# Optimization experiments

Measured on AMD Instinct MI355X. Metric: run time of the kernel, lower is better.

Reference implementation:

```python
import jax, jax.numpy as jnp
import numpy as np
from jax import lax

B, L = 2, 1024
D_MODEL, D_STATE, EXPAND, D_CONV = 1024, 16, 2, 4
D_INNER = EXPAND * D_MODEL            # 2048
DT_RANK = (D_MODEL + 15) // 16        # 64


def setup_inputs() -> dict:
    key = jax.random.key(0)
    ks = jax.random.split(key, 8)
    g = lambda k, shape, s=0.02: jax.random.normal(k, shape, dtype=jnp.float32) * s
    # Mamba-style A init: A = -exp(A_log), A_log = log(1..d_state) per channel
    A_log = jnp.log(jnp.broadcast_to(
        jnp.arange(1, D_STATE + 1, dtype=jnp.float32), (D_INNER, D_STATE)))
    return {
        "x": jax.random.normal(ks[0], (B, L, D_MODEL), dtype=jnp.float32),
        "W_in": g(ks[1], (D_MODEL, 2 * D_INNER)),
        "conv_w": g(ks[2], (D_INNER, D_CONV), 0.1),
        "conv_b": jnp.zeros((D_INNER,), jnp.float32),
        "W_x": g(ks[3], (D_INNER, DT_RANK + 2 * D_STATE)),
        "W_dt": g(ks[4], (DT_RANK, D_INNER)),
        "b_dt": g(ks[5], (D_INNER,), 0.1),
        "A_log": A_log,
        "D_skip": jnp.ones((D_INNER,), jnp.float32),
        "W_out": g(ks[6], (D_INNER, D_MODEL)),
    }


def reference(x, W_in, conv_w, conv_b, W_x, W_dt, b_dt, A_log, D_skip, W_out):
    # in_proj -> (u, z): [B, L, D_INNER] each
    xz = x @ W_in
    u, z = xz[..., :D_INNER], xz[..., D_INNER:]

    # causal depthwise conv1d, kernel D_CONV (small fixed loop over taps)
    up = jnp.pad(u, ((0, 0), (D_CONV - 1, 0), (0, 0)))
    u = sum(up[:, k:k + L, :] * conv_w[:, k] for k in range(D_CONV)) + conv_b
    u = jax.nn.silu(u)

    # input-dependent dt, B, C
    x_dbl = u @ W_x                                    # [B, L, dt_rank + 2N]
    dt = x_dbl[..., :DT_RANK]
    Bm = x_dbl[..., DT_RANK:DT_RANK + D_STATE]         # [B, L, N]
    Cm = x_dbl[..., DT_RANK + D_STATE:]                # [B, L, N]
    delta = jax.nn.softplus(dt @ W_dt + b_dt)          # [B, L, D]

    A = -jnp.exp(A_log)                                # [D, N]
    deltaA = jnp.exp(jnp.einsum('bld,dn->bldn', delta, A))   # [B, L, D, N]
    dBu = (delta * u)[..., None] * Bm[:, :, None, :]          # [B, L, D, N]

    def step(h, inp):
        dA_t, dBu_t, c_t = inp                         # [B,D,N],[B,D,N],[B,N]
        h = dA_t * h + dBu_t
        y_t = jnp.einsum('bdn,bn->bd', h, c_t)
        return h, y_t

    h0 = jnp.zeros((B, D_INNER, D_STATE), x.dtype)
    _, ys = lax.scan(step, h0,
                     (deltaA.transpose(1, 0, 2, 3),
                      dBu.transpose(1, 0, 2, 3),
                      Cm.transpose(1, 0, 2)))
    y = ys.transpose(1, 0, 2) + u * D_skip             # [B, L, D_INNER]
    y = y * jax.nn.silu(z)                             # gated output
    return y @ W_out                                   # [B, L, D_MODEL]
```

## Files before the change

### kernel.cpp

```cpp
#include <hip/hip_runtime.h>


typedef unsigned short u16;
typedef unsigned int   u32;

#define B_SZ 2
#define L_SZ 1024
#define DM   1024
#define DI   2048
#define DS   16
#define DTR  64
#define NXD  96
#define NCHUNK 16
#define CL   64
#define KSPLIT 8
#define KC     256
#define OSPLIT 4

typedef __bf16 bf16x8 __attribute__((ext_vector_type(8)));
typedef float  f32x4  __attribute__((ext_vector_type(4)));

__device__ __forceinline__ u16 f2bf(float f) {
    u32 x = __float_as_uint(f);
    x += 0x7fffu + ((x >> 16) & 1u);
    return (u16)(x >> 16);
}

__device__ __forceinline__ void gld_lds16(const u16* g, u16* l) {
    __builtin_amdgcn_global_load_lds(
        (const __attribute__((address_space(1))) u32*)g,
        (__attribute__((address_space(3))) u32*)l, 16, 0, 0);
}

__global__ __launch_bounds__(256) void gemm128u2(
    const u16* __restrict__ A, const u16* __restrict__ BT,
    float* __restrict__ C, const float* __restrict__ bias,
    int M, int N, int K, int KCHUNK, int op)
{
    __shared__ u16 As0[128 * 32];
    __shared__ u16 Bs0[128 * 32];
    __shared__ u16 As1[128 * 32];
    __shared__ u16 Bs1[128 * 32];

    const int tid  = threadIdx.x;
    const int wave = tid >> 6;
    const int lane = tid & 63;
    const int q    = lane >> 4;
    const int r16  = lane & 15;
    const int wm   = (wave & 1) * 64;
    const int wn   = (wave >> 1) * 64;
    const int m0   = blockIdx.y * 128;
    const int n0   = blockIdx.x * 128;
    const int srow = tid >> 2;
    const int sseg = (tid & 3) * 8;
    const int kb   = blockIdx.z * KCHUNK;

    const u16* gA0 = A  + (size_t)(m0 + srow)      * K + sseg;
    const u16* gA1 = A  + (size_t)(m0 + 64 + srow) * K + sseg;
    const u16* gB0 = BT + (size_t)(n0 + srow)      * K + sseg;
    const u16* gB1 = BT + (size_t)(n0 + 64 + srow) * K + sseg;
    u16* lA0 = As0 + tid * 8;  u16* lA0b = As0 + 2048 + tid * 8;
    u16* lB0 = Bs0 + tid * 8;  u16* lB0b = Bs0 + 2048 + tid * 8;
    u16* lA1 = As1 + tid * 8;  u16* lA1b = As1 + 2048 + tid * 8;
    u16* lB1 = Bs1 + tid * 8;  u16* lB1b = Bs1 + 2048 + tid * 8;

    f32x4 acc[4][4];
#pragma unroll
    for (int s = 0; s < 4; ++s)
#pragma unroll
        for (int j = 0; j < 4; ++j) acc[s][j] = (f32x4){0.f, 0.f, 0.f, 0.f};

    for (int k0 = kb; k0 < kb + KCHUNK; k0 += 64) {
        __syncthreads();
        gld_lds16(gA0 + k0, lA0);
        gld_lds16(gA1 + k0, lA0b);
        gld_lds16(gB0 + k0, lB0);
        gld_lds16(gB1 + k0, lB0b);
        gld_lds16(gA0 + k0 + 32, lA1);
        gld_lds16(gA1 + k0 + 32, lA1b);
        gld_lds16(gB0 + k0 + 32, lB1);
        gld_lds16(gB1 + k0 + 32, lB1b);
        __syncthreads();

        bf16x8 af[4], bfr[4];
#pragma unroll
        for (int s = 0; s < 4; ++s)
            af[s] = *(const bf16x8*)(As0 + (wm + s * 16 + r16) * 32 + q * 8);
#pragma unroll
        for (int j = 0; j < 4; ++j)
            bfr[j] = *(const bf16x8*)(Bs0 + (wn + j * 16 + r16) * 32 + q * 8);
#pragma unroll
        for (int s = 0; s < 4; ++s)
#pragma unroll
            for (int j = 0; j < 4; ++j)
                acc[s][j] = __builtin_amdgcn_mfma_f32_16x16x32_bf16(
                    af[s], bfr[j], acc[s][j], 0, 0, 0);
#pragma unroll
        for (int s = 0; s < 4; ++s)
            af[s] = *(const bf16x8*)(As1 + (wm + s * 16 + r16) * 32 + q * 8);
#pragma unroll
        for (int j = 0; j < 4; ++j)
            bfr[j] = *(const bf16x8*)(Bs1 + (wn + j * 16 + r16) * 32 + q * 8);
#pragma unroll
        for (int s = 0; s < 4; ++s)
#pragma unroll
            for (int j = 0; j < 4; ++j)
                acc[s][j] = __builtin_amdgcn_mfma_f32_16x16x32_bf16(
                    af[s], bfr[j], acc[s][j], 0, 0, 0);
    }

    float* Cz = C + (size_t)blockIdx.z * M * N;
#pragma unroll
    for (int s = 0; s < 4; ++s) {
        const int row0 = m0 + wm + s * 16 + q * 4;
#pragma unroll
        for (int j = 0; j < 4; ++j) {
            const int col = n0 + wn + j * 16 + r16;
            if (op == 1) {
                const float bv = bias[col];
#pragma unroll
                for (int i = 0; i < 4; ++i) {
                    float v = acc[s][j][i] + bv;
                    v = (v > 20.f) ? v : log1pf(__expf(v));
                    Cz[(size_t)(row0 + i) * N + col] = v;
                }
            } else {
#pragma unroll
                for (int i = 0; i < 4; ++i)
                    Cz[(size_t)(row0 + i) * N + col] = acc[s][j][i];
            }
        }
    }
}

__global__ __launch_bounds__(256) void reduce_out(
    const float* __restrict__ part, float* __restrict__ out, int n)
{
    const int i = (blockIdx.x * 256 + threadIdx.x) * 4;
    if (i >= n) return;
    f32x4 v = *(const f32x4*)(part + i);
#pragma unroll
    for (int s = 1; s < OSPLIT; ++s) {
        f32x4 p = *(const f32x4*)(part + (size_t)s * n + i);
        v.x += p.x; v.y += p.y; v.z += p.z; v.w += p.w;
    }
    *(f32x4*)(out + i) = v;
}

__global__ __launch_bounds__(256) void gemm_skinny_splitk(
    const u16* __restrict__ A, const u16* __restrict__ BT,
    float* __restrict__ Cpart, int M, int N, int K)
{
    constexpr int LDT = 40;
    __shared__ u16 As[128 * LDT];
    __shared__ u16 Bs[64 * LDT];

    const int tid  = threadIdx.x;
    const int wave = tid >> 6;
    const int lane = tid & 63;
    const int q    = lane >> 4;
    const int r16  = lane & 15;
    const int m0   = blockIdx.y * 128;
    const int n0   = blockIdx.x * 64;
    const int kcs  = blockIdx.z * KC;
    const int sr   = tid >> 2;
    const int ss   = (tid & 3) * 8;

    f32x4 acc[2][4];
#pragma unroll
    for (int s = 0; s < 2; ++s)
#pragma unroll
        for (int j = 0; j < 4; ++j) acc[s][j] = (f32x4){0.f, 0.f, 0.f, 0.f};

    const int  bcol   = n0 + sr;
    const bool bvalid = bcol < N;

    for (int k0 = kcs; k0 < kcs + KC; k0 += 32) {
        __syncthreads();
        uint4 a0 = *(const uint4*)(A + (size_t)(m0 + sr)      * K + k0 + ss);
        uint4 a1 = *(const uint4*)(A + (size_t)(m0 + 64 + sr) * K + k0 + ss);
        uint4 bv = make_uint4(0u, 0u, 0u, 0u);
        if (bvalid) bv = *(const uint4*)(BT + (size_t)bcol * K + k0 + ss);
        *(uint4*)(As + sr * LDT + ss)        = a0;
        *(uint4*)(As + (64 + sr) * LDT + ss) = a1;
        *(uint4*)(Bs + sr * LDT + ss)        = bv;
        __syncthreads();

        bf16x8 af[2], bfr[4];
#pragma unroll
        for (int s = 0; s < 2; ++s)
            af[s] = *(const bf16x8*)(As + (wave * 32 + s * 16 + r16) * LDT + q * 8);
#pragma unroll
        for (int j = 0; j < 4; ++j)
            bfr[j] = *(const bf16x8*)(Bs + (j * 16 + r16) * LDT + q * 8);
#pragma unroll
        for (int s = 0; s < 2; ++s)
#pragma unroll
            for (int j = 0; j < 4; ++j)
                acc[s][j] = __builtin_amdgcn_mfma_f32_16x16x32_bf16(
                    af[s], bfr[j], acc[s][j], 0, 0, 0);
    }

    float* Cp = Cpart + (size_t)blockIdx.z * M * N;
#pragma unroll
    for (int s = 0; s < 2; ++s) {
        const int row0 = m0 + wave * 32 + s * 16 + q * 4;
#pragma unroll
        for (int j = 0; j < 4; ++j) {
            const int col = n0 + j * 16 + r16;
            if (col < N) {
#pragma unroll
                for (int i = 0; i < 4; ++i)
                    Cp[(size_t)(row0 + i) * N + col] = acc[s][j][i];
            }
        }
    }
}

__global__ __launch_bounds__(256) void reduce_xdbl(
    const float* __restrict__ part, float* __restrict__ xdbl,
    u16* __restrict__ dtbf)
{
    const int i = blockIdx.x * 256 + threadIdx.x;
    const int row = i / NXD, col = i - row * NXD;
    float v = 0.f;
#pragma unroll
    for (int s = 0; s < KSPLIT; ++s)
        v += part[(size_t)s * (B_SZ * L_SZ * NXD) + i];
    xdbl[i] = v;
    if (col < DTR) dtbf[row * DTR + col] = f2bf(v);
}

__device__ __forceinline__ void tr_tile(
    const float* __restrict__ in, u16* __restrict__ out,
    int R, int C, int tr, int tc, int tid, float (*t)[33])
{
    const int tx = tid & 31, ty = tid >> 5;
    const int r0 = tr * 32, c0 = tc * 32;
#pragma unroll
    for (int i = 0; i < 4; ++i) {
        int r = r0 + ty + i * 8, c = c0 + tx;
        if (r < R && c < C) t[ty + i * 8][tx] = in[(size_t)r * C + c];
    }
    __syncthreads();
#pragma unroll
    for (int i = 0; i < 4; ++i) {
        int oR = c0 + ty + i * 8, oC = r0 + tx;
        if (oR < C && oC < R) out[(size_t)oR * R + oC] = f2bf(t[tx][ty + i * 8]);
    }
}

__global__ __launch_bounds__(256) void prep_kernel(
    const float* __restrict__ x,     u16* __restrict__ xbf,
    const float* __restrict__ W_in,  u16* __restrict__ winT,
    const float* __restrict__ W_out, u16* __restrict__ woutT,
    const float* __restrict__ W_x,   u16* __restrict__ wxT,
    const float* __restrict__ W_dt,  u16* __restrict__ wdtT)
{
    __shared__ float t[32][33];
    const int id  = blockIdx.x;
    const int tid = threadIdx.x;
    if (id < 4096) {
        tr_tile(W_in, winT, 1024, 4096, id >> 7, id & 127, tid, t);
    } else if (id < 6144) {
        int i2 = id - 4096;
        tr_tile(W_out, woutT, 2048, 1024, i2 >> 5, i2 & 31, tid, t);
    } else if (id < 6336) {
        int i3 = id - 6144;
        tr_tile(W_x, wxT, 2048, 96, i3 / 3, i3 % 3, tid, t);
    } else if (id < 6464) {
        int i4 = id - 6336;
        tr_tile(W_dt, wdtT, 64, 2048, i4 >> 6, i4 & 63, tid, t);
    } else {
        int i = (id - 6464) * 256 + tid;
        xbf[i] = f2bf(x[i]);
    }
}

__global__ __launch_bounds__(256) void conv_silu_kernel(
    const float* __restrict__ xz, const float* __restrict__ cw,
    const float* __restrict__ cb, float* __restrict__ uc, u16* __restrict__ ucbf)
{
    const int idx = blockIdx.x * 256 + threadIdx.x;
    const int d   = idx & (DI - 1);
    const int pos = idx >> 11;
    const int l   = pos & (L_SZ - 1);
    float s = cb[d];
#pragma unroll
    for (int k = 0; k < 4; ++k) {
        int ls = l + k - 3;
        if (ls >= 0)
            s = fmaf(xz[(size_t)(pos + k - 3) * (2 * DI) + d], cw[d * 4 + k], s);
    }
    float v = s / (1.f + __expf(-s));
    uc[idx]   = v;
    ucbf[idx] = f2bf(v);
}

__global__ __launch_bounds__(256) void scan_pass1(
    const float* __restrict__ delta, const float* __restrict__ uc,
    const float* __restrict__ xdbl, const float* __restrict__ A_log,
    float* __restrict__ hbuf, float* __restrict__ pbuf)
{
    const int c = blockIdx.x;
    const int d = blockIdx.y * 256 + threadIdx.x;
    const int b = blockIdx.z;
    float Av[16], h[16], P[16];
#pragma unroll
    for (int n = 0; n < 16; ++n) {
        Av[n] = -__expf(A_log[d * 16 + n]);
        h[n] = 0.f; P[n] = 1.f;
    }
    const int rowbase = b * L_SZ + c * CL;
    for (int i = 0; i < CL; ++i) {
        const int row = rowbase + i;
        float dlt = delta[(size_t)row * DI + d];
        float uu  = uc[(size_t)row * DI + d];
        float du  = dlt * uu;
        const float* xr = xdbl + (size_t)row * NXD;
#pragma unroll
        for (int n = 0; n < 16; ++n) {
            float e = __expf(dlt * Av[n]);
            P[n] *= e;
            h[n] = fmaf(e, h[n], du * xr[DTR + n]);
        }
    }
    size_t base = ((size_t)((b * NCHUNK + c) * DI + d)) * 16;
#pragma unroll
    for (int n = 0; n < 16; ++n) { hbuf[base + n] = h[n]; pbuf[base + n] = P[n]; }
}

__global__ __launch_bounds__(256) void scan_pass2(
    float* __restrict__ hbuf, const float* __restrict__ pbuf)
{
    const int j = blockIdx.x * 256 + threadIdx.x;
    const int b = blockIdx.y;
    float h0 = 0.f;
    for (int cc = 0; cc < NCHUNK; ++cc) {
        size_t o = ((size_t)(b * NCHUNK + cc)) * (DI * 16) + j;
        float hl = hbuf[o];
        float Pl = pbuf[o];
        hbuf[o] = h0;
        h0 = fmaf(Pl, h0, hl);
    }
}

__global__ __launch_bounds__(256) void scan_pass3(
    const float* __restrict__ delta, const float* __restrict__ uc,
    const float* __restrict__ xdbl, const float* __restrict__ A_log,
    const float* __restrict__ hbuf, const float* __restrict__ xz,
    const float* __restrict__ Dskip, u16* __restrict__ ybf)
{
    const int c = blockIdx.x;
    const int d = blockIdx.y * 256 + threadIdx.x;
    const int b = blockIdx.z;
    float Av[16], h[16];
    size_t base = ((size_t)((b * NCHUNK + c) * DI + d)) * 16;
#pragma unroll
    for (int n = 0; n < 16; ++n) {
        Av[n] = -__expf(A_log[d * 16 + n]);
        h[n]  = hbuf[base + n];
    }
    const float Dk = Dskip[d];
    const int rowbase = b * L_SZ + c * CL;
    for (int i = 0; i < CL; ++i) {
        const int row = rowbase + i;
        float dlt = delta[(size_t)row * DI + d];
        float uu  = uc[(size_t)row * DI + d];
        float du  = dlt * uu;
        const float* xr = xdbl + (size_t)row * NXD;
        float y = 0.f;
#pragma unroll
        for (int n = 0; n < 16; ++n) {
            float e = __expf(dlt * Av[n]);
            h[n] = fmaf(e, h[n], du * xr[DTR + n]);
            y = fmaf(h[n], xr[DTR + DS + n], y);
        }
        float zz = xz[(size_t)row * (2 * DI) + DI + d];
        float yv = fmaf(uu, Dk, y) * (zz / (1.f + __expf(-zz)));
        ybf[(size_t)row * DI + d] = f2bf(yv);
    }
}

constexpr size_t OFF_XZ      = 0;
constexpr size_t OFF_UC      = OFF_XZ    + 8388608;
constexpr size_t OFF_DELTA   = OFF_UC    + 4194304;
constexpr size_t OFF_XDBL    = OFF_DELTA + 4194304;
constexpr size_t OFF_SCRATCH = OFF_XDBL  + 196608;
constexpr size_t OFF_F32_END = OFF_SCRATCH + 4194304;
constexpr size_t SOFF_XBF   = 0;
constexpr size_t SOFF_WINT  = SOFF_XBF   + 2097152;
constexpr size_t SOFF_UCBF  = SOFF_WINT  + 4194304;
constexpr size_t SOFF_WXT   = SOFF_UCBF  + 4194304;
constexpr size_t SOFF_DTBF  = SOFF_WXT   + 196608;
constexpr size_t SOFF_WDTT  = SOFF_DTBF  + 131072;
constexpr size_t SOFF_WOUTT = SOFF_WDTT  + 131072;
constexpr size_t SOFF_YBF   = SOFF_WOUTT + 2097152;

extern "C" void kernel_launch(void* const* d_in, const int* in_sizes, int n_in,
                              void* d_out, int out_size, void* d_ws, size_t ws_size,
                              hipStream_t stream)
{
    const float* x     = (const float*)d_in[0];
    const float* W_in  = (const float*)d_in[1];
    const float* cw    = (const float*)d_in[2];
    const float* cb    = (const float*)d_in[3];
    const float* W_x   = (const float*)d_in[4];
    const float* W_dt  = (const float*)d_in[5];
    const float* b_dt  = (const float*)d_in[6];
    const float* A_log = (const float*)d_in[7];
    const float* Dsk   = (const float*)d_in[8];
    const float* W_out = (const float*)d_in[9];
    float* out = (float*)d_out;

    float* wsf   = (float*)d_ws;
    float* xz    = wsf + OFF_XZ;
    float* opart = wsf + OFF_XZ;
    float* uc    = wsf + OFF_UC;
    float* dlt   = wsf + OFF_DELTA;
    float* xdbl  = wsf + OFF_XDBL;
    float* xpart = wsf + OFF_SCRATCH;
    float* hbuf  = wsf + OFF_SCRATCH;
    float* pbuf  = wsf + OFF_SCRATCH + 2097152;
    u16* sb    = (u16*)(wsf + OFF_F32_END);
    u16* xbf   = sb + SOFF_XBF;
    u16* winT  = sb + SOFF_WINT;
    u16* ucbf  = sb + SOFF_UCBF;
    u16* wxT   = sb + SOFF_WXT;
    u16* dtbf  = sb + SOFF_DTBF;
    u16* wdtT  = sb + SOFF_WDTT;
    u16* woutT = sb + SOFF_WOUTT;
    u16* ybf   = sb + SOFF_YBF;

    prep_kernel<<<14656, 256, 0, stream>>>(x, xbf, W_in, winT, W_out, woutT,
                                           W_x, wxT, W_dt, wdtT);

    gemm128u2<<<dim3(4096 / 128, 2048 / 128, 1), 256, 0, stream>>>(
        xbf, winT, xz, nullptr, 2048, 4096, 1024, 1024, 0);

    conv_silu_kernel<<<(B_SZ * L_SZ * DI) / 256, 256, 0, stream>>>(xz, cw, cb, uc, ucbf);

    gemm_skinny_splitk<<<dim3(2, 2048 / 128, KSPLIT), 256, 0, stream>>>(
        ucbf, wxT, xpart, 2048, NXD, 2048);
    reduce_xdbl<<<(B_SZ * L_SZ * NXD) / 256, 256, 0, stream>>>(xpart, xdbl, dtbf);

    gemm128u2<<<dim3(2048 / 128, 2048 / 128, 1), 256, 0, stream>>>(
        dtbf, wdtT, dlt, b_dt, 2048, 2048, 64, 64, 1);

    scan_pass1<<<dim3(NCHUNK, DI / 256, B_SZ), 256, 0, stream>>>(dlt, uc, xdbl, A_log, hbuf, pbuf);
    scan_pass2<<<dim3(DI * 16 / 256, B_SZ), 256, 0, stream>>>(hbuf, pbuf);
    scan_pass3<<<dim3(NCHUNK, DI / 256, B_SZ), 256, 0, stream>>>(dlt, uc, xdbl, A_log, hbuf, xz, Dsk, ybf);

    gemm128u2<<<dim3(1024 / 128, 2048 / 128, OSPLIT), 256, 0, stream>>>(
        ybf, woutT, opart, nullptr, 2048, 1024, 2048, 2048 / OSPLIT, 0);
    reduce_out<<<(2048 * 1024 / 4 + 255) / 256, 256, 0, stream>>>(
        opart, out, 2048 * 1024);
}
```

Before: 278.8 us.

## Fuse three-pass chunked scan with decoupled lookback and store xz, u in bf16

Merges the three scan kernels into one, where each chunk block waits on a flag from the previous chunk and reads its carried state. This removes the separate carry-propagation kernel, one recomputation launch, and the hbuf/pbuf round trips. The in_proj GEMM now writes xz as bf16, and the fp32 copy of the conv output is dropped, so the scan reads bf16 u and z, roughly halving that traffic. The cost is a serial dependency across the 16 chunks, which could deadlock if blocks are not scheduled in order, plus lower precision for u and z.

Result: slower. 679.9 us (+143.9%).

```diff
diff --git a/kernel.cpp b/kernel.cpp
--- a/kernel.cpp
+++ b/kernel.cpp
@@ -25,6 +25,9 @@
     x += 0x7fffu + ((x >> 16) & 1u);
     return (u16)(x >> 16);
 }
+__device__ __forceinline__ float bf2f(u16 v) {
+    return __uint_as_float(((u32)v) << 16);
+}
 
 __device__ __forceinline__ void gld_lds16(const u16* g, u16* l) {
     __builtin_amdgcn_global_load_lds(
@@ -34,7 +37,8 @@
 
 __global__ __launch_bounds__(256) void gemm128u2(
     const u16* __restrict__ A, const u16* __restrict__ BT,
-    float* __restrict__ C, const float* __restrict__ bias,
+    float* __restrict__ Cf, u16* __restrict__ Cb,
+    const float* __restrict__ bias,
     int M, int N, int K, int KCHUNK, int op)
 {
     __shared__ u16 As0[128 * 32];
@@ -109,25 +113,29 @@
                     af[s], bfr[j], acc[s][j], 0, 0, 0);
     }
 
-    float* Cz = C + (size_t)blockIdx.z * M * N;
 #pragma unroll
     for (int s = 0; s < 4; ++s) {
         const int row0 = m0 + wm + s * 16 + q * 4;
 #pragma unroll
         for (int j = 0; j < 4; ++j) {
             const int col = n0 + wn + j * 16 + r16;
-            if (op == 1) {
+            if (op == 0) {
+                float* Cz = Cf + (size_t)blockIdx.z * M * N;
+#pragma unroll
+                for (int i = 0; i < 4; ++i)
+                    Cz[(size_t)(row0 + i) * N + col] = acc[s][j][i];
+            } else if (op == 1) {
                 const float bv = bias[col];
 #pragma unroll
                 for (int i = 0; i < 4; ++i) {
                     float v = acc[s][j][i] + bv;
                     v = (v > 20.f) ? v : log1pf(__expf(v));
-                    Cz[(size_t)(row0 + i) * N + col] = v;
+                    Cf[(size_t)(row0 + i) * N + col] = v;
                 }
             } else {
 #pragma unroll
                 for (int i = 0; i < 4; ++i)
-                    Cz[(size_t)(row0 + i) * N + col] = acc[s][j][i];
+                    Cb[(size_t)(row0 + i) * N + col] = f2bf(acc[s][j][i]);
             }
         }
     }
@@ -255,7 +263,8 @@
     const float* __restrict__ W_in,  u16* __restrict__ winT,
     const float* __restrict__ W_out, u16* __restrict__ woutT,
     const float* __restrict__ W_x,   u16* __restrict__ wxT,
-    const float* __restrict__ W_dt,  u16* __restrict__ wdtT)
+    const float* __restrict__ W_dt,  u16* __restrict__ wdtT,
+    int* __restrict__ flags)
 {
     __shared__ float t[32][33];
     const int id  = blockIdx.x;
@@ -271,15 +280,17 @@
     } else if (id < 6464) {
         int i4 = id - 6336;
         tr_tile(W_dt, wdtT, 64, 2048, i4 >> 6, i4 & 63, tid, t);
-    } else {
+    } else if (id < 14656) {
         int i = (id - 6464) * 256 + tid;
         xbf[i] = f2bf(x[i]);
+    } else {
+        flags[tid] = 0;
     }
 }
 
 __global__ __launch_bounds__(256) void conv_silu_kernel(
-    const float* __restrict__ xz, const float* __restrict__ cw,
-    const float* __restrict__ cb, float* __restrict__ uc, u16* __restrict__ ucbf)
+    const u16* __restrict__ xzbf, const float* __restrict__ cw,
+    const float* __restrict__ cb, u16* __restrict__ ucbf)
 {
     const int idx = blockIdx.x * 256 + threadIdx.x;
     const int d   = idx & (DI - 1);
@@ -290,32 +301,38 @@
     for (int k = 0; k < 4; ++k) {
         int ls = l + k - 3;
         if (ls >= 0)
-            s = fmaf(xz[(size_t)(pos + k - 3) * (2 * DI) + d], cw[d * 4 + k], s);
+            s = fmaf(bf2f(xzbf[(size_t)(pos + k - 3) * (2 * DI) + d]), cw[d * 4 + k], s);
     }
     float v = s / (1.f + __expf(-s));
-    uc[idx]   = v;
     ucbf[idx] = f2bf(v);
 }
 
-__global__ __launch_bounds__(256) void scan_pass1(
-    const float* __restrict__ delta, const float* __restrict__ uc,
+__global__ __launch_bounds__(256) void scan_fused(
+    const float* __restrict__ delta, const u16* __restrict__ ucbf,
     const float* __restrict__ xdbl, const float* __restrict__ A_log,
-    float* __restrict__ hbuf, float* __restrict__ pbuf)
-{
-    const int c = blockIdx.x;
-    const int d = blockIdx.y * 256 + threadIdx.x;
-    const int b = blockIdx.z;
+    const u16* __restrict__ xzbf, const float* __restrict__ Dskip,
+    float* __restrict__ carry, int* __restrict__ flags,
+    u16* __restrict__ ybf)
+{
+    const int c   = blockIdx.x;
+    const int g   = blockIdx.y;
+    const int b   = blockIdx.z;
+    const int tid = threadIdx.x;
+    const int d   = g * 256 + tid;
+    const int chain = b * 8 + g;
+
     float Av[16], h[16], P[16];
 #pragma unroll
     for (int n = 0; n < 16; ++n) {
         Av[n] = -__expf(A_log[d * 16 + n]);
         h[n] = 0.f; P[n] = 1.f;
     }
+
     const int rowbase = b * L_SZ + c * CL;
     for (int i = 0; i < CL; ++i) {
         const int row = rowbase + i;
         float dlt = delta[(size_t)row * DI + d];
-        float uu  = uc[(size_t)row * DI + d];
+        float uu  = bf2f(ucbf[(size_t)row * DI + d]);
         float du  = dlt * uu;
         const float* xr = xdbl + (size_t)row * NXD;
 #pragma unroll
@@ -325,48 +342,43 @@
             h[n] = fmaf(e, h[n], du * xr[DTR + n]);
         }
     }
-    size_t base = ((size_t)((b * NCHUNK + c) * DI + d)) * 16;
-#pragma unroll
-    for (int n = 0; n < 16; ++n) { hbuf[base + n] = h[n]; pbuf[base + n] = P[n]; }
-}
-
-__global__ __launch_bounds__(256) void scan_pass2(
-    float* __restrict__ hbuf, const float* __restrict__ pbuf)
-{
-    const int j = blockIdx.x * 256 + threadIdx.x;
-    const int b = blockIdx.y;
-    float h0 = 0.f;
-    for (int cc = 0; cc < NCHUNK; ++cc) {
-        size_t o = ((size_t)(b * NCHUNK + cc)) * (DI * 16) + j;
-        float hl = hbuf[o];
-        float Pl = pbuf[o];
-        hbuf[o] = h0;
-        h0 = fmaf(Pl, h0, hl);
-    }
-}
-
-__global__ __launch_bounds__(256) void scan_pass3(
-    const float* __restrict__ delta, const float* __restrict__ uc,
-    const float* __restrict__ xdbl, const float* __restrict__ A_log,
-    const float* __restrict__ hbuf, const float* __restrict__ xz,
-    const float* __restrict__ Dskip, u16* __restrict__ ybf)
-{
-    const int c = blockIdx.x;
-    const int d = blockIdx.y * 256 + threadIdx.x;
-    const int b = blockIdx.z;
-    float Av[16], h[16];
-    size_t base = ((size_t)((b * NCHUNK + c) * DI + d)) * 16;
-#pragma unroll
-    for (int n = 0; n < 16; ++n) {
-        Av[n] = -__expf(A_log[d * 16 + n]);
-        h[n]  = hbuf[base + n];
-    }
+
+    float h0[16];
+    if (c == 0) {
+#pragma unroll
+        for (int n = 0; n < 16; ++n) h0[n] = 0.f;
+    } else {
+        if (tid == 0) {
+            while (__hip_atomic_load(&flags[chain * NCHUNK + (c - 1)],
+                                     __ATOMIC_ACQUIRE, __HIP_MEMORY_SCOPE_AGENT) == 0)
+                __builtin_amdgcn_s_sleep(2);
+        }
+        __syncthreads();
+        const float* cp = carry +
+            (((size_t)(chain * NCHUNK + (c - 1)) * 256 + tid) * 16);
+#pragma unroll
+        for (int n = 0; n < 16; ++n)
+            h0[n] = __hip_atomic_load(cp + n, __ATOMIC_RELAXED, __HIP_MEMORY_SCOPE_AGENT);
+    }
+    if (c < NCHUNK - 1) {
+        float* co = carry + (((size_t)(chain * NCHUNK + c) * 256 + tid) * 16);
+#pragma unroll
+        for (int n = 0; n < 16; ++n)
+            co[n] = fmaf(P[n], h0[n], h[n]);
+        __threadfence();
+        __syncthreads();
+        if (tid == 0)
+            __hip_atomic_store(&flags[chain * NCHUNK + c], 1,
+                               __ATOMIC_RELEASE, __HIP_MEMORY_SCOPE_AGENT);
+    }
+
+#pragma unroll
+    for (int n = 0; n < 16; ++n) h[n] = h0[n];
     const float Dk = Dskip[d];
-    const int rowbase = b * L_SZ + c * CL;
     for (int i = 0; i < CL; ++i) {
         const int row = rowbase + i;
         float dlt = delta[(size_t)row * DI + d];
-        float uu  = uc[(size_t)row * DI + d];
+        float uu  = bf2f(ucbf[(size_t)row * DI + d]);
         float du  = dlt * uu;
         const float* xr = xdbl + (size_t)row * NXD;
         float y = 0.f;
@@ -376,21 +388,22 @@
             h[n] = fmaf(e, h[n], du * xr[DTR + n]);
             y = fmaf(h[n], xr[DTR + DS + n], y);
         }
-        float zz = xz[(size_t)row * (2 * DI) + DI + d];
+        float zz = bf2f(xzbf[(size_t)row * (2 * DI) + DI + d]);
         float yv = fmaf(uu, Dk, y) * (zz / (1.f + __expf(-zz)));
         ybf[(size_t)row * DI + d] = f2bf(yv);
     }
 }
 
-constexpr size_t OFF_XZ      = 0;
-constexpr size_t OFF_UC      = OFF_XZ    + 8388608;
-constexpr size_t OFF_DELTA   = OFF_UC    + 4194304;
+constexpr size_t OFF_DELTA   = 0;
 constexpr size_t OFF_XDBL    = OFF_DELTA + 4194304;
 constexpr size_t OFF_SCRATCH = OFF_XDBL  + 196608;
-constexpr size_t OFF_F32_END = OFF_SCRATCH + 4194304;
+constexpr size_t OFF_F32_END = OFF_SCRATCH + 8388608;
+constexpr size_t SCR_CARRY   = 2097152;
+constexpr size_t SCR_FLAGS   = 3145728;
 constexpr size_t SOFF_XBF   = 0;
 constexpr size_t SOFF_WINT  = SOFF_XBF   + 2097152;
-constexpr size_t SOFF_UCBF  = SOFF_WINT  + 4194304;
+constexpr size_t SOFF_XZBF  = SOFF_WINT  + 4194304;
+constexpr size_t SOFF_UCBF  = SOFF_XZBF  + 8388608;
 constexpr size_t SOFF_WXT   = SOFF_UCBF  + 4194304;
 constexpr size_t SOFF_DTBF  = SOFF_WXT   + 196608;
 constexpr size_t SOFF_WDTT  = SOFF_DTBF  + 131072;
@@ -414,17 +427,16 @@
     float* out = (float*)d_out;
 
     float* wsf   = (float*)d_ws;
-    float* xz    = wsf + OFF_XZ;
-    float* opart = wsf + OFF_XZ;
-    float* uc    = wsf + OFF_UC;
     float* dlt   = wsf + OFF_DELTA;
     float* xdbl  = wsf + OFF_XDBL;
     float* xpart = wsf + OFF_SCRATCH;
-    float* hbuf  = wsf + OFF_SCRATCH;
-    float* pbuf  = wsf + OFF_SCRATCH + 2097152;
+    float* carry = wsf + OFF_SCRATCH + SCR_CARRY;
+    int*   flags = (int*)(wsf + OFF_SCRATCH + SCR_FLAGS);
+    float* opart = wsf + OFF_SCRATCH;
     u16* sb    = (u16*)(wsf + OFF_F32_END);
     u16* xbf   = sb + SOFF_XBF;
     u16* winT  = sb + SOFF_WINT;
+    u16* xzbf  = sb + SOFF_XZBF;
     u16* ucbf  = sb + SOFF_UCBF;
     u16* wxT   = sb + SOFF_WXT;
     u16* dtbf  = sb + SOFF_DTBF;
@@ -432,27 +444,26 @@
     u16* woutT = sb + SOFF_WOUTT;
     u16* ybf   = sb + SOFF_YBF;
 
-    prep_kernel<<<14656, 256, 0, stream>>>(x, xbf, W_in, winT, W_out, woutT,
-                                           W_x, wxT, W_dt, wdtT);
-
-    gemm128u2<<<dim3(4096 / 128, 2048 / 128, 1), 256, 0, stream>>>(
-        xbf, winT, xz, nullptr, 2048, 4096, 1024, 1024, 0);
-
-    conv_silu_kernel<<<(B_SZ * L_SZ * DI) / 256, 256, 0, stream>>>(xz, cw, cb, uc, ucbf);
-
-    gemm_skinny_splitk<<<dim3(2, 2048 / 128, KSPLIT), 256, 0, stream>>>(
+    prep_kernel<<<14657, 256, 0, stream>>>(x, xbf, W_in, winT, W_out, woutT,
+                                           W_x, wxT, W_dt, wdtT, flags);
+
+    gemm128u2<<<dim3(32, 16, 1), 256, 0, stream>>>(
+        xbf, winT, nullptr, xzbf, nullptr, 2048, 4096, 1024, 1024, 2);
+
+    conv_silu_kernel<<<(B_SZ * L_SZ * DI) / 256, 256, 0, stream>>>(xzbf, cw, cb, ucbf);
+
+    gemm_skinny_splitk<<<dim3(2, 16, KSPLIT), 256, 0, stream>>>(
         ucbf, wxT, xpart, 2048, NXD, 2048);
     reduce_xdbl<<<(B_SZ * L_SZ * NXD) / 256, 256, 0, stream>>>(xpart, xdbl, dtbf);
 
-    gemm128u2<<<dim3(2048 / 128, 2048 / 128, 1), 256, 0, stream>>>(
-        dtbf, wdtT, dlt, b_dt, 2048, 2048, 64, 64, 1);
-
-    scan_pass1<<<dim3(NCHUNK, DI / 256, B_SZ), 256, 0, stream>>>(dlt, uc, xdbl, A_log, hbuf, pbuf);
-    scan_pass2<<<dim3(DI * 16 / 256, B_SZ), 256, 0, stream>>>(hbuf, pbuf);
-    scan_pass3<<<dim3(NCHUNK, DI / 256, B_SZ), 256, 0, stream>>>(dlt, uc, xdbl, A_log, hbuf, xz, Dsk, ybf);
-
-    gemm128u2<<<dim3(1024 / 128, 2048 / 128, OSPLIT), 256, 0, stream>>>(
-        ybf, woutT, opart, nullptr, 2048, 1024, 2048, 2048 / OSPLIT, 0);
+    gemm128u2<<<dim3(16, 16, 1), 256, 0, stream>>>(
+        dtbf, wdtT, dlt, nullptr, b_dt, 2048, 2048, 64, 64, 1);
+
+    scan_fused<<<dim3(NCHUNK, DI / 256, B_SZ), 256, 0, stream>>>(
+        dlt, ucbf, xdbl, A_log, xzbf, Dsk, carry, flags, ybf);
+
+    gemm128u2<<<dim3(8, 16, OSPLIT), 256, 0, stream>>>(
+        ybf, woutT, opart, nullptr, nullptr, 2048, 1024, 2048, 2048 / OSPLIT, 0);
     reduce_out<<<(2048 * 1024 / 4 + 255) / 256, 256, 0, stream>>>(
         opart, out, 2048 * 1024);
 }
```
